# Optimization experiments

Hardware: AMD Instinct MI355X
Metric: run time of the kernel (lower is better)

The kernel has to match this reference:

```python
import jax, jax.numpy as jnp
import numpy as np

B, S, D, H = 2, 2048, 1024, 16
DK = D // H
LARGE = 1e9
LN_EPS = 1e-5


def sinusoidal_embeddings(seq_len, d):
    pos = jnp.arange(seq_len, dtype=jnp.float32)[:, None]          # [S,1]
    i = jnp.arange(d // 2, dtype=jnp.float32)[None, :]             # [1,d/2]
    freq = jnp.exp(-(2.0 * i / d) * jnp.log(10000.0))
    ang = pos * freq                                               # [S,d/2]
    pe = jnp.zeros((seq_len, d), dtype=jnp.float32)
    pe = pe.at[:, 0::2].set(jnp.sin(ang))
    pe = pe.at[:, 1::2].set(jnp.cos(ang))
    return pe


def setup_inputs() -> dict:
    key = jax.random.key(0)
    ks = jax.random.split(key, 6)
    sc = 1.0 / np.sqrt(D)
    return {
        "X": jax.random.normal(ks[0], (B, S, D), jnp.float32),
        "W_q": jax.random.normal(ks[1], (D, D), jnp.float32) * sc,
        "W_k": jax.random.normal(ks[2], (D, D), jnp.float32) * sc,
        "W_v": jax.random.normal(ks[3], (D, D), jnp.float32) * sc,
        "W_o": jax.random.normal(ks[4], (D, D), jnp.float32) * sc,
        "alpha": jnp.ones((1, H, S - 1, 1), jnp.float32),
        "ln_scale": jnp.ones((D,), jnp.float32),
        "ln_bias": jnp.zeros((D,), jnp.float32),
    }


def reference(X, W_q, W_k, W_v, W_o, alpha, ln_scale, ln_bias):
    # projections (torch Linear: x @ W.T), split heads -> [B,H,S,dk]
    def proj(W):
        return jnp.einsum('bsd,ed->bse', X, W).reshape(B, S, H, DK).transpose(0, 2, 1, 3)
    Q, K, V = proj(W_q), proj(W_k), proj(W_v)

    # EMA smear on K along sequence
    a = jax.nn.sigmoid(alpha)                                      # [1,H,S-1,1]
    smeared = K[:, :, 1:, :] * a + K[:, :, :-1, :] * (1.0 - a)
    K = jnp.concatenate([K[:, :, 0:1, :], smeared], axis=2)

    # inline sinusoidal positional embeddings added to K and Q
    pe = sinusoidal_embeddings(S, DK)                              # [S,dk]
    K = K + pe
    Q = Q + pe

    mask = jnp.triu(jnp.ones((S, S), jnp.float32), k=1) * (-LARGE)
    scores = jnp.einsum('bhqd,bhkd->bhqk', Q, K) / jnp.sqrt(jnp.float32(DK)) + mask
    weights = jax.nn.softmax(scores, axis=-1)
    attn = jnp.einsum('bhqk,bhkd->bhqd', weights, V)               # [B,H,S,dk]
    attn = attn.transpose(0, 2, 1, 3).reshape(B, S, D)

    Y = jnp.einsum('bsd,ed->bse', attn, W_o) + X

    # LayerNorm
    mu = jnp.mean(Y, axis=-1, keepdims=True)
    var = jnp.mean(jnp.square(Y - mu), axis=-1, keepdims=True)
    Y = (Y - mu) / jnp.sqrt(var + LN_EPS) * ln_scale + ln_bias
    return Y
```

## Files before the change

kernel.cpp:

```cpp
#include <hip/hip_runtime.h>


#define LB __launch_bounds__(256)

typedef unsigned short u16;
typedef unsigned int u32;
typedef __attribute__((ext_vector_type(2))) unsigned int u32x2;
typedef __attribute__((ext_vector_type(4))) unsigned short us4;
typedef __attribute__((ext_vector_type(8))) unsigned short us8;
typedef __attribute__((ext_vector_type(8))) __bf16 bf8;
typedef __attribute__((ext_vector_type(4))) float f4;
typedef __attribute__((ext_vector_type(4))) short s4;

#define QSCALE 0.18033688011112042f

#if __has_builtin(__builtin_amdgcn_exp2f)
#define EXP2 __builtin_amdgcn_exp2f
#else
#define EXP2 exp2f
#endif

static __device__ __forceinline__ float bf2f(u16 h) {
  union { unsigned int u; float f; } c; c.u = ((unsigned int)h) << 16; return c.f;
}
static __device__ __forceinline__ u16 f2bf(float f) {
  union { float f; unsigned int u; } c; c.f = f;
  unsigned int u = c.u + 0x7FFFu + ((c.u >> 16) & 1u);
  return (u16)(u >> 16);
}
#if __has_builtin(__builtin_amdgcn_cvt_pk_bf16_f32)
typedef __attribute__((ext_vector_type(2))) __bf16 bf2v;
static __device__ __forceinline__ us4 pk_bf16x4(f4 v) {
  bf2v lo = __builtin_amdgcn_cvt_pk_bf16_f32(v[0], v[1]);
  bf2v hi = __builtin_amdgcn_cvt_pk_bf16_f32(v[2], v[3]);
  u32x2 r = {__builtin_bit_cast(u32, lo), __builtin_bit_cast(u32, hi)};
  return __builtin_bit_cast(us4, r);
}
#else
static __device__ __forceinline__ us4 pk_bf16x4(f4 v) {
  return us4{f2bf(v[0]), f2bf(v[1]), f2bf(v[2]), f2bf(v[3])};
}
#endif
static __device__ __forceinline__ float pe_val(int s, int dk) {
  float fr = __expf((float)(dk & ~1) * (-9.210340371976184f / 64.0f));
  float ang = (float)s * fr;
  return (dk & 1) ? __cosf(ang) : __sinf(ang);
}

#if __has_builtin(__builtin_amdgcn_mfma_f32_16x16x16bf16_1k)
static __device__ __forceinline__ f4 mfma16(us4 a, us4 b, f4 c) {
  return __builtin_amdgcn_mfma_f32_16x16x16bf16_1k(
      __builtin_bit_cast(s4, a), __builtin_bit_cast(s4, b), c, 0, 0, 0);
}
#elif __has_builtin(__builtin_amdgcn_mfma_f32_16x16x16_bf16)
typedef __attribute__((ext_vector_type(4))) __bf16 bf4;
static __device__ __forceinline__ f4 mfma16(us4 a, us4 b, f4 c) {
  return __builtin_amdgcn_mfma_f32_16x16x16_bf16(
      __builtin_bit_cast(bf4, a), __builtin_bit_cast(bf4, b), c, 0, 0, 0);
}
#else
static __device__ __forceinline__ f4 mfma16(us4 a, us4 b, f4 c) {
  asm volatile("v_mfma_f32_16x16x16_bf16 %0, %1, %2, %0" : "+v"(c) : "v"(a), "v"(b));
  return c;
}
#endif

#define GLDS(gp, lp) __builtin_amdgcn_global_load_lds( \
    (const __attribute__((address_space(1))) void*)(gp), \
    (__attribute__((address_space(3))) void*)(lp), 16, 0, 0)

__global__ LB void cvt_kernel(const float* __restrict__ X, const float* __restrict__ Wq,
                              const float* __restrict__ Wk, const float* __restrict__ Wv,
                              const float* __restrict__ Wo, u16* __restrict__ Xb,
                              u16* __restrict__ Wcat, u16* __restrict__ Wob) {
  const unsigned t = blockIdx.x * 256 + threadIdx.x;
  const float* src; u16* dst; size_t off;
  if (t < (512u << 10))      { src = X;  dst = Xb;                off = t; }
  else if (t < (640u << 10)) { src = Wq; dst = Wcat;              off = t - (512u << 10); }
  else if (t < (768u << 10)) { src = Wk; dst = Wcat + (1u << 20); off = t - (640u << 10); }
  else if (t < (896u << 10)) { src = Wv; dst = Wcat + (2u << 20); off = t - (768u << 10); }
  else                       { src = Wo; dst = Wob;               off = t - (896u << 10); }
  off *= 8;
  f4 a = *(const f4*)(src + off);
  f4 b = *(const f4*)(src + off + 4);
  us8 o = {f2bf(a[0]), f2bf(a[1]), f2bf(a[2]), f2bf(a[3]),
           f2bf(b[0]), f2bf(b[1]), f2bf(b[2]), f2bf(b[3])};
  *(us8*)(dst + off) = o;
}

static __device__ __forceinline__ void gemm_core(
    const u16* __restrict__ Abase, const u16* __restrict__ Bbase,
    u16* Als, u16* Bls, int m0, int n0, int tid, f4 acc[4][4]) {
  const int w = tid >> 6, lane = tid & 63;
  const int l16 = lane & 15, quad = lane >> 4;
  const int wm = w & 1, wn = w >> 1;
  for (int kk = 0; kk < 1024; kk += 32) {
    __syncthreads();
#pragma unroll
    for (int it = 0; it < 2; it++) {
      int cb = (w * 2 + it) * 64;
      int c = cb + lane;
      int row = c >> 2, kc = c & 3;
      GLDS(Abase + (size_t)(m0 + row) * 1024 + kk + kc * 8, &Als[cb * 8]);
      GLDS(Bbase + (size_t)(n0 + row) * 1024 + kk + kc * 8, &Bls[cb * 8]);
    }
    __syncthreads();
    bf8 af[4], bfr[4];
#pragma unroll
    for (int mt = 0; mt < 4; mt++)
      af[mt] = __builtin_bit_cast(bf8, *(const us8*)(&Als[(wm * 64 + mt * 16 + l16) * 32 + quad * 8]));
#pragma unroll
    for (int nt = 0; nt < 4; nt++)
      bfr[nt] = __builtin_bit_cast(bf8, *(const us8*)(&Bls[(wn * 64 + nt * 16 + l16) * 32 + quad * 8]));
#pragma unroll
    for (int mt = 0; mt < 4; mt++)
#pragma unroll
      for (int nt = 0; nt < 4; nt++)
        acc[mt][nt] = __builtin_amdgcn_mfma_f32_16x16x32_bf16(af[mt], bfr[nt], acc[mt][nt], 0, 0, 0);
  }
}

__global__ LB void gemm_qkv(const u16* __restrict__ Xb, const u16* __restrict__ Wcat,
                            u16* __restrict__ Qb, u16* __restrict__ Kraw,
                            u16* __restrict__ Vp) {
  __shared__ u16 Als[128 * 32];
  __shared__ u16 Bls[128 * 32];
  const int tid = threadIdx.x;
  const int m0 = blockIdx.y * 128, n0 = blockIdx.x * 128;
  f4 acc[4][4];
#pragma unroll
  for (int a = 0; a < 4; a++)
#pragma unroll
    for (int b = 0; b < 4; b++) acc[a][b] = f4{0.f, 0.f, 0.f, 0.f};
  gemm_core(Xb, Wcat, Als, Bls, m0, n0, tid, acc);

  const int w = tid >> 6, lane = tid & 63;
  const int l16 = lane & 15, quad = lane >> 4;
  const int wm = w & 1, wn = w >> 1;
  const int z = blockIdx.x >> 3;
  if (z == 2) {
    const int b = m0 >> 11;
    const int hh = ((n0 + wn * 64) & 1023) >> 6;
    const size_t bhoff = (size_t)(b * 16 + hh) * (2048 * 64);
#pragma unroll
    for (int mt = 0; mt < 4; mt++) {
      int sb = (m0 & 2047) + wm * 64 + mt * 16;
      int kb = sb >> 6;
      int t  = (sb >> 4) & 3;
#pragma unroll
      for (int nt = 0; nt < 4; nt++) {
        size_t o = bhoff + (size_t)kb * 4096 +
                   (size_t)(((t * 4 + nt) * 64 + quad * 16 + l16) * 4);
        *(us4*)(Vp + o) = pk_bf16x4(acc[mt][nt]);
      }
    }
  } else {
#pragma unroll
    for (int mt = 0; mt < 4; mt++)
#pragma unroll
      for (int nt = 0; nt < 4; nt++)
#pragma unroll
        for (int r = 0; r < 4; r++) {
          int m = m0 + wm * 64 + mt * 16 + quad * 4 + r;
          int nn = (n0 + wn * 64 + nt * 16 + l16) & 1023;
          float v = acc[mt][nt][r];
          int b = m >> 11, s = m & 2047, h = nn >> 6, dk = nn & 63;
          size_t bhoff = (size_t)(b * 16 + h) * (2048 * 64);
          if (z == 0) {
            Qb[bhoff + (size_t)s * 64 + dk] = f2bf((v + pe_val(s, dk)) * QSCALE);
          } else {
            Kraw[bhoff + (size_t)s * 64 + dk] = f2bf(v);
          }
        }
  }
}

__global__ LB void ema_pe(const u16* __restrict__ Kraw, const float* __restrict__ alpha,
                          u16* __restrict__ Kp) {
  int idx = blockIdx.x * 256 + threadIdx.x;
  int b8  = idx & 7;
  int s   = (idx >> 3) & 2047;
  int bh  = idx >> 14;
  int dk8 = b8 * 8;
  size_t base = ((size_t)bh * 2048 + s) * 64 + dk8;
  us8 kc = *(const us8*)(Kraw + base);
  float kv[8];
#pragma unroll
  for (int j = 0; j < 8; j++) kv[j] = bf2f(kc[j]);
  if (s > 0) {
    us8 kp = *(const us8*)(Kraw + base - 64);
    float aa = alpha[(bh & 15) * 2047 + s - 1];
    float a = 1.0f / (1.0f + __expf(-aa));
#pragma unroll
    for (int j = 0; j < 8; j++) kv[j] = kv[j] * a + bf2f(kp[j]) * (1.0f - a);
  }
  us8 o;
#pragma unroll
  for (int j = 0; j < 8; j++) o[j] = f2bf(kv[j] + pe_val(s, dk8 + j));
  int kt16 = s >> 4, c = b8 >> 2, quad = b8 & 3, l16s = s & 15;
  size_t off = (size_t)bh * (2048 * 64) + (size_t)kt16 * 1024 + (c * 64 + quad * 16 + l16s) * 8;
  *(us8*)(Kp + off) = o;
}

template<bool MASK>
static __device__ __forceinline__ void attn_step(
    int kb, const u16* __restrict__ Kt, const u16* __restrict__ Vt,
    const bf8* qf, f4* acc, float& lsum, int lane, int quad, int qrel0) {
  const u16* kbase = Kt + (size_t)kb * 4096;
  const u16* vbase = Vt + (size_t)kb * 4096;
  f4 sc[4];
#pragma unroll
  for (int t = 0; t < 4; t++) sc[t] = f4{0.f, 0.f, 0.f, 0.f};
#pragma unroll
  for (int t = 0; t < 4; t++)
#pragma unroll
    for (int c = 0; c < 2; c++) {
      bf8 kf = __builtin_bit_cast(bf8, *(const us8*)(kbase + (t * 2 + c) * 512 + lane * 8));
      sc[t] = __builtin_amdgcn_mfma_f32_16x16x32_bf16(kf, qf[c], sc[t], 0, 0, 0);
    }
  us4 pf[4];
#pragma unroll
  for (int t = 0; t < 4; t++) {
    f4 pv;
#pragma unroll
    for (int r = 0; r < 4; r++) {
      float s = sc[t][r];
      if (MASK && (t * 16 + quad * 4 + r > qrel0)) s = -1e30f;
      float p = EXP2(s);
      lsum += p;
      pv[r] = p;
    }
    pf[t] = pk_bf16x4(pv);
  }
#pragma unroll
  for (int t = 0; t < 4; t++)
#pragma unroll
    for (int dn = 0; dn < 4; dn++) {
      us4 vf = *(const us4*)(vbase + ((t * 4 + dn) * 64 + lane) * 4);
      acc[dn] = mfma16(vf, pf[t], acc[dn]);
    }
}

__global__ LB void attn_kernel(const u16* __restrict__ Qb, const u16* __restrict__ Kp,
                               const u16* __restrict__ Vp, u16* __restrict__ Ab) {
  __shared__ float comb[3][64][20];
  const int tid = threadIdx.x, w = tid >> 6, lane = tid & 63;
  const int l16 = lane & 15, quad = lane >> 4;
  const int idx = blockIdx.x;
  const int bh = idx & 31;
  const int qtile = 127 - (idx >> 5);
  const int qw = qtile * 16;
  const size_t bhoff = (size_t)bh * (2048 * 64);
  const u16* Kt = Kp + bhoff;
  const u16* Vt = Vp + bhoff;

  bf8 qf[2];
#pragma unroll
  for (int c = 0; c < 2; c++)
    qf[c] = __builtin_bit_cast(bf8, *(const us8*)(Qb + bhoff + (size_t)(qw + l16) * 64 + c * 32 + quad * 8));

  f4 acc[4];
#pragma unroll
  for (int dn = 0; dn < 4; dn++) acc[dn] = f4{0.f, 0.f, 0.f, 0.f};
  float lsum = 0.f;

  const int T   = (qw >> 6) + 1;
  const int kbs = (w * T) >> 2;
  const int kbe = ((w + 1) * T) >> 2;
  const int e_un = (kbe < T - 1) ? kbe : (T - 1);
  for (int kb = kbs; kb < e_un; kb++)
    attn_step<false>(kb, Kt, Vt, qf, acc, lsum, lane, quad, 0);
  if (kbe == T && kbe > kbs)
    attn_step<true>(T - 1, Kt, Vt, qf, acc, lsum, lane, quad, qw + l16 - (T - 1) * 64);

  if (w) {
    float* d = &comb[w - 1][lane][0];
    *(f4*)(d)      = acc[0];
    *(f4*)(d + 4)  = acc[1];
    *(f4*)(d + 8)  = acc[2];
    *(f4*)(d + 12) = acc[3];
    d[16] = lsum;
  }
  __syncthreads();
  if (w == 0) {
#pragma unroll
    for (int i = 0; i < 3; i++) {
      const float* s = &comb[i][lane][0];
      acc[0] += *(const f4*)(s);
      acc[1] += *(const f4*)(s + 4);
      acc[2] += *(const f4*)(s + 8);
      acc[3] += *(const f4*)(s + 12);
      lsum += s[16];
    }
    lsum += __shfl_xor(lsum, 16, 64);
    lsum += __shfl_xor(lsum, 32, 64);
    float rinv = 1.0f / lsum;
    const int b = bh >> 4, h = bh & 15;
    const int q = qw + l16;
    u16* orow = Ab + ((size_t)(b * 2048 + q)) * 1024 + h * 64;
#pragma unroll
    for (int dn = 0; dn < 4; dn++) {
      us4 o = pk_bf16x4(f4{acc[dn][0] * rinv, acc[dn][1] * rinv,
                           acc[dn][2] * rinv, acc[dn][3] * rinv});
      *(us4*)(orow + dn * 16 + quad * 4) = o;
    }
  }
}

__global__ LB void gemm_out(const u16* __restrict__ Ab, const u16* __restrict__ Wob,
                            const float* __restrict__ X, float* __restrict__ Yp) {
  __shared__ u16 Als[128 * 32];
  __shared__ u16 Bls[128 * 32];
  const int tid = threadIdx.x;
  const int m0 = blockIdx.y * 128, n0 = blockIdx.x * 128;
  f4 acc[4][4];
#pragma unroll
  for (int a = 0; a < 4; a++)
#pragma unroll
    for (int b = 0; b < 4; b++) acc[a][b] = f4{0.f, 0.f, 0.f, 0.f};
  gemm_core(Ab, Wob, Als, Bls, m0, n0, tid, acc);

  const int w = tid >> 6, lane = tid & 63;
  const int l16 = lane & 15, quad = lane >> 4;
  const int wm = w & 1, wn = w >> 1;
#pragma unroll
  for (int mt = 0; mt < 4; mt++)
#pragma unroll
    for (int nt = 0; nt < 4; nt++)
#pragma unroll
      for (int r = 0; r < 4; r++) {
        int m = m0 + wm * 64 + mt * 16 + quad * 4 + r;
        int n = n0 + wn * 64 + nt * 16 + l16;
        size_t o = (size_t)m * 1024 + n;
        Yp[o] = acc[mt][nt][r] + X[o];
      }
}

__global__ LB void ln_kernel(const float* __restrict__ Y, const float* __restrict__ g,
                             const float* __restrict__ bta, float* __restrict__ out) {
  __shared__ float ls[4], lsq[4];
  const int row = blockIdx.x, tid = threadIdx.x;
  const int w = tid >> 6, lane = tid & 63;
  f4 v = *(const f4*)(Y + (size_t)row * 1024 + tid * 4);
  float s  = v[0] + v[1] + v[2] + v[3];
  float sq = v[0] * v[0] + v[1] * v[1] + v[2] * v[2] + v[3] * v[3];
#pragma unroll
  for (int d = 1; d < 64; d <<= 1) { s += __shfl_xor(s, d, 64); sq += __shfl_xor(sq, d, 64); }
  if (lane == 0) { ls[w] = s; lsq[w] = sq; }
  __syncthreads();
  s  = ls[0] + ls[1] + ls[2] + ls[3];
  sq = lsq[0] + lsq[1] + lsq[2] + lsq[3];
  float mu  = s * (1.0f / 1024.0f);
  float var = sq * (1.0f / 1024.0f) - mu * mu;
  float rs  = rsqrtf(var + 1e-5f);
  f4 o;
#pragma unroll
  for (int j = 0; j < 4; j++) {
    int col = tid * 4 + j;
    o[j] = (v[j] - mu) * rs * g[col] + bta[col];
  }
  *(f4*)(out + (size_t)row * 1024 + tid * 4) = o;
}

extern "C" void kernel_launch(void* const* d_in, const int* in_sizes, int n_in,
                              void* d_out, int out_size, void* d_ws, size_t ws_size,
                              hipStream_t stream) {
  (void)in_sizes; (void)n_in; (void)out_size; (void)ws_size;
  const float* X  = (const float*)d_in[0];
  const float* Wq = (const float*)d_in[1];
  const float* Wk = (const float*)d_in[2];
  const float* Wv = (const float*)d_in[3];
  const float* Wo = (const float*)d_in[4];
  const float* al = (const float*)d_in[5];
  const float* g  = (const float*)d_in[6];
  const float* bt = (const float*)d_in[7];

  char* ws = (char*)d_ws;
  float* Yp   = (float*)(ws);
  u16*   Xb   = (u16*)(ws + ((size_t)16 << 20));
  u16*   Wcat = (u16*)(ws + ((size_t)24 << 20));
  u16*   Wob  = (u16*)(ws + ((size_t)30 << 20));
  u16*   Qb   = (u16*)(ws + ((size_t)32 << 20));
  u16*   Kraw = (u16*)(ws + ((size_t)40 << 20));
  u16*   Ab   = (u16*)(ws + ((size_t)40 << 20));
  u16*   Kp   = (u16*)(ws + ((size_t)48 << 20));
  u16*   Vp   = (u16*)(ws + ((size_t)56 << 20));

  cvt_kernel<<<dim3(4096), 256, 0, stream>>>(X, Wq, Wk, Wv, Wo, Xb, Wcat, Wob);
  gemm_qkv<<<dim3(24, 32), 256, 0, stream>>>(Xb, Wcat, Qb, Kraw, Vp);
  ema_pe<<<dim3(2048), 256, 0, stream>>>(Kraw, al, Kp);
  attn_kernel<<<dim3(4096), 256, 0, stream>>>(Qb, Kp, Vp, Ab);
  gemm_out<<<dim3(8, 32), 256, 0, stream>>>(Ab, Wob, X, Yp);
  ln_kernel<<<dim3(4096), 256, 0, stream>>>(Yp, g, bt, (float*)d_out);
}
```

Before: 227.6 us.

## Process two 16-row query tiles per attention block to reuse K/V loads

Each attention block now handles 32 query rows (two 16-row MFMA tiles) instead of 16. Every K and V fragment loaded from global memory feeds MFMAs for both tiles, halving K/V traffic per query and halving the grid. The cost is doubled accumulator and score registers, which may lower occupancy, plus fewer blocks for load balancing across the causal triangle. The mask offset is shifted by 16 for the second tile so causality is preserved.

```diff
diff --git a/kernel.cpp b/kernel.cpp
--- a/kernel.cpp
+++ b/kernel.cpp
@@ -203,106 +203,127 @@
 }
 
 template<bool MASK>
-static __device__ __forceinline__ void attn_step(
+static __device__ __forceinline__ void attn_step2(
     int kb, const u16* __restrict__ Kt, const u16* __restrict__ Vt,
-    const bf8* qf, f4* acc, float& lsum, int lane, int quad, int qrel0) {
+    const bf8 qf[2][2], f4 acc[2][4], float* lsum, int lane, int quad, int qrel0) {
   const u16* kbase = Kt + (size_t)kb * 4096;
   const u16* vbase = Vt + (size_t)kb * 4096;
-  f4 sc[4];
-#pragma unroll
-  for (int t = 0; t < 4; t++) sc[t] = f4{0.f, 0.f, 0.f, 0.f};
+  f4 sc[2][4];
+#pragma unroll
+  for (int h = 0; h < 2; h++)
+#pragma unroll
+    for (int t = 0; t < 4; t++) sc[h][t] = f4{0.f, 0.f, 0.f, 0.f};
 #pragma unroll
   for (int t = 0; t < 4; t++)
 #pragma unroll
     for (int c = 0; c < 2; c++) {
       bf8 kf = __builtin_bit_cast(bf8, *(const us8*)(kbase + (t * 2 + c) * 512 + lane * 8));
-      sc[t] = __builtin_amdgcn_mfma_f32_16x16x32_bf16(kf, qf[c], sc[t], 0, 0, 0);
-    }
-  us4 pf[4];
-#pragma unroll
-  for (int t = 0; t < 4; t++) {
-    f4 pv;
-#pragma unroll
-    for (int r = 0; r < 4; r++) {
-      float s = sc[t][r];
-      if (MASK && (t * 16 + quad * 4 + r > qrel0)) s = -1e30f;
-      float p = EXP2(s);
-      lsum += p;
-      pv[r] = p;
-    }
-    pf[t] = pk_bf16x4(pv);
-  }
+      sc[0][t] = __builtin_amdgcn_mfma_f32_16x16x32_bf16(kf, qf[0][c], sc[0][t], 0, 0, 0);
+      sc[1][t] = __builtin_amdgcn_mfma_f32_16x16x32_bf16(kf, qf[1][c], sc[1][t], 0, 0, 0);
+    }
+  us4 pf[2][4];
+#pragma unroll
+  for (int h = 0; h < 2; h++)
+#pragma unroll
+    for (int t = 0; t < 4; t++) {
+      f4 pv;
+#pragma unroll
+      for (int r = 0; r < 4; r++) {
+        float s = sc[h][t][r];
+        if (MASK && (t * 16 + quad * 4 + r > qrel0 + h * 16)) s = -1e30f;
+        float p = EXP2(s);
+        lsum[h] += p;
+        pv[r] = p;
+      }
+      pf[h][t] = pk_bf16x4(pv);
+    }
 #pragma unroll
   for (int t = 0; t < 4; t++)
 #pragma unroll
     for (int dn = 0; dn < 4; dn++) {
       us4 vf = *(const us4*)(vbase + ((t * 4 + dn) * 64 + lane) * 4);
-      acc[dn] = mfma16(vf, pf[t], acc[dn]);
+      acc[0][dn] = mfma16(vf, pf[0][t], acc[0][dn]);
+      acc[1][dn] = mfma16(vf, pf[1][t], acc[1][dn]);
     }
 }
 
 __global__ LB void attn_kernel(const u16* __restrict__ Qb, const u16* __restrict__ Kp,
                                const u16* __restrict__ Vp, u16* __restrict__ Ab) {
-  __shared__ float comb[3][64][20];
+  __shared__ float comb[3][64][36];
   const int tid = threadIdx.x, w = tid >> 6, lane = tid & 63;
   const int l16 = lane & 15, quad = lane >> 4;
   const int idx = blockIdx.x;
   const int bh = idx & 31;
-  const int qtile = 127 - (idx >> 5);
-  const int qw = qtile * 16;
+  const int qg = 63 - (idx >> 5);
+  const int qw = qg * 32;
   const size_t bhoff = (size_t)bh * (2048 * 64);
   const u16* Kt = Kp + bhoff;
   const u16* Vt = Vp + bhoff;
 
-  bf8 qf[2];
-#pragma unroll
-  for (int c = 0; c < 2; c++)
-    qf[c] = __builtin_bit_cast(bf8, *(const us8*)(Qb + bhoff + (size_t)(qw + l16) * 64 + c * 32 + quad * 8));
-
-  f4 acc[4];
-#pragma unroll
-  for (int dn = 0; dn < 4; dn++) acc[dn] = f4{0.f, 0.f, 0.f, 0.f};
-  float lsum = 0.f;
+  bf8 qf[2][2];
+#pragma unroll
+  for (int h = 0; h < 2; h++)
+#pragma unroll
+    for (int c = 0; c < 2; c++)
+      qf[h][c] = __builtin_bit_cast(bf8,
+          *(const us8*)(Qb + bhoff + (size_t)(qw + h * 16 + l16) * 64 + c * 32 + quad * 8));
+
+  f4 acc[2][4];
+#pragma unroll
+  for (int h = 0; h < 2; h++)
+#pragma unroll
+    for (int dn = 0; dn < 4; dn++) acc[h][dn] = f4{0.f, 0.f, 0.f, 0.f};
+  float lsum[2] = {0.f, 0.f};
 
   const int T   = (qw >> 6) + 1;
   const int kbs = (w * T) >> 2;
   const int kbe = ((w + 1) * T) >> 2;
   const int e_un = (kbe < T - 1) ? kbe : (T - 1);
   for (int kb = kbs; kb < e_un; kb++)
-    attn_step<false>(kb, Kt, Vt, qf, acc, lsum, lane, quad, 0);
+    attn_step2<false>(kb, Kt, Vt, qf, acc, lsum, lane, quad, 0);
   if (kbe == T && kbe > kbs)
-    attn_step<true>(T - 1, Kt, Vt, qf, acc, lsum, lane, quad, qw + l16 - (T - 1) * 64);
+    attn_step2<true>(T - 1, Kt, Vt, qf, acc, lsum, lane, quad, qw + l16 - (T - 1) * 64);
 
   if (w) {
     float* d = &comb[w - 1][lane][0];
-    *(f4*)(d)      = acc[0];
-    *(f4*)(d + 4)  = acc[1];
-    *(f4*)(d + 8)  = acc[2];
-    *(f4*)(d + 12) = acc[3];
-    d[16] = lsum;
+#pragma unroll
+    for (int h = 0; h < 2; h++)
+#pragma unroll
+      for (int dn = 0; dn < 4; dn++)
+        *(f4*)(d + (h * 4 + dn) * 4) = acc[h][dn];
+    d[32] = lsum[0];
+    d[33] = lsum[1];
   }
   __syncthreads();
   if (w == 0) {
 #pragma unroll
     for (int i = 0; i < 3; i++) {
       const float* s = &comb[i][lane][0];
-      acc[0] += *(const f4*)(s);
-      acc[1] += *(const f4*)(s + 4);
-      acc[2] += *(const f4*)(s + 8);
-      acc[3] += *(const f4*)(s + 12);
-      lsum += s[16];
-    }
-    lsum += __shfl_xor(lsum, 16, 64);
-    lsum += __shfl_xor(lsum, 32, 64);
-    float rinv = 1.0f / lsum;
-    const int b = bh >> 4, h = bh & 15;
-    const int q = qw + l16;
-    u16* orow = Ab + ((size_t)(b * 2048 + q)) * 1024 + h * 64;
-#pragma unroll
-    for (int dn = 0; dn < 4; dn++) {
-      us4 o = pk_bf16x4(f4{acc[dn][0] * rinv, acc[dn][1] * rinv,
-                           acc[dn][2] * rinv, acc[dn][3] * rinv});
-      *(us4*)(orow + dn * 16 + quad * 4) = o;
+#pragma unroll
+      for (int h = 0; h < 2; h++)
+#pragma unroll
+        for (int dn = 0; dn < 4; dn++)
+          acc[h][dn] += *(const f4*)(s + (h * 4 + dn) * 4);
+      lsum[0] += s[32];
+      lsum[1] += s[33];
+    }
+#pragma unroll
+    for (int h = 0; h < 2; h++) {
+      lsum[h] += __shfl_xor(lsum[h], 16, 64);
+      lsum[h] += __shfl_xor(lsum[h], 32, 64);
+    }
+    const int b = bh >> 4, hd = bh & 15;
+#pragma unroll
+    for (int h = 0; h < 2; h++) {
+      float rinv = 1.0f / lsum[h];
+      const int q = qw + h * 16 + l16;
+      u16* orow = Ab + ((size_t)(b * 2048 + q)) * 1024 + hd * 64;
+#pragma unroll
+      for (int dn = 0; dn < 4; dn++) {
+        us4 o = pk_bf16x4(f4{acc[h][dn][0] * rinv, acc[h][dn][1] * rinv,
+                             acc[h][dn][2] * rinv, acc[h][dn][3] * rinv});
+        *(us4*)(orow + dn * 16 + quad * 4) = o;
+      }
     }
   }
 }
@@ -389,7 +410,7 @@
   cvt_kernel<<<dim3(4096), 256, 0, stream>>>(X, Wq, Wk, Wv, Wo, Xb, Wcat, Wob);
   gemm_qkv<<<dim3(24, 32), 256, 0, stream>>>(Xb, Wcat, Qb, Kraw, Vp);
   ema_pe<<<dim3(2048), 256, 0, stream>>>(Kraw, al, Kp);
-  attn_kernel<<<dim3(4096), 256, 0, stream>>>(Qb, Kp, Vp, Ab);
+  attn_kernel<<<dim3(2048), 256, 0, stream>>>(Qb, Kp, Vp, Ab);
   gemm_out<<<dim3(8, 32), 256, 0, stream>>>(Ab, Wob, X, Yp);
   ln_kernel<<<dim3(4096), 256, 0, stream>>>(Yp, g, bt, (float*)d_out);
 }
```

After: 239.9 us. +5.4%, slower.
